# Kernel optimization log

Hardware: AMD Instinct MI355X
Metric: run time of the kernel (lower is better)

## Reference

```python
import jax, jax.numpy as jnp
import numpy as np

N_NODES = 100000
N_EDGES = 3200000
IN_DIM = 32
HID = 64


def setup_inputs() -> dict:
    key = jax.random.key(0)
    ks = jax.random.split(key, 10)
    x = jax.random.normal(ks[0], (N_NODES, IN_DIM), dtype=jnp.float32)
    edge_index = jax.random.randint(ks[1], (2, N_EDGES), 0, N_NODES, dtype=jnp.int64)
    s = 0.1
    return {
        "x": x,
        "edge_index": edge_index,
        # SAGEConv layer 1: lin_l (neighbor path, with bias), lin_r (root path, no bias)
        "w1_l": jax.random.normal(ks[2], (HID, IN_DIM), dtype=jnp.float32) * s,
        "b1_l": jnp.zeros((HID,), dtype=jnp.float32),
        "w1_r": jax.random.normal(ks[3], (HID, IN_DIM), dtype=jnp.float32) * s,
        # SAGEConv layer 2
        "w2_l": jax.random.normal(ks[4], (HID, HID), dtype=jnp.float32) * s,
        "b2_l": jnp.zeros((HID,), dtype=jnp.float32),
        "w2_r": jax.random.normal(ks[5], (HID, HID), dtype=jnp.float32) * s,
        # final classifier Linear(hidden, 1)
        "w_cls": jax.random.normal(ks[6], (1, HID), dtype=jnp.float32) * s,
        "b_cls": jnp.zeros((1,), dtype=jnp.float32),
    }


def _sage_conv(h, src, dst, n_nodes, w_l, b_l, w_r):
    # mean-aggregate neighbor features (src -> dst), then lin_l(agg) + lin_r(h)
    msg = h[src]                                   # [E, F] gather
    agg = jax.ops.segment_sum(msg, dst, num_segments=n_nodes)
    cnt = jax.ops.segment_sum(jnp.ones((src.shape[0],), h.dtype), dst,
                              num_segments=n_nodes)
    mean = agg / jnp.maximum(cnt, 1.0)[:, None]    # [N, F]
    return mean @ w_l.T + b_l + h @ w_r.T


def reference(x, edge_index, w1_l, b1_l, w1_r, w2_l, b2_l, w2_r, w_cls, b_cls):
    src, dst = edge_index[0], edge_index[1]
    n = x.shape[0]
    h = _sage_conv(x, src, dst, n, w1_l, b1_l, w1_r)
    h = jax.nn.relu(h)  # dropout is identity at inference
    h = _sage_conv(h, src, dst, n, w2_l, b2_l, w2_r)
    h = jax.nn.relu(h)
    logits = h @ w_cls.T + b_cls                   # [N, 1]
    return jnp.squeeze(logits, -1)                 # [N]
```

## Files before the change

### kernel.cpp

```cpp
#include <hip/hip_runtime.h>

#define N_NODES 100000
#define N_EDGES 3200000
#define IN_DIM 32
#define HID 64
#define BSHIFT 8
#define BNODES 256
#define NB ((N_NODES + BNODES - 1) / BNODES)
#define NWG 256
#define CHUNK (N_EDGES / NWG)
#define XBLOCKS ((N_NODES * IN_DIM + 255) / 256)

typedef unsigned short u16;
typedef unsigned char u8;
typedef _Float16 h2 __attribute__((ext_vector_type(2)));
typedef _Float16 half8 __attribute__((ext_vector_type(8)));
typedef float float4v __attribute__((ext_vector_type(4)));
typedef float f32x2 __attribute__((ext_vector_type(2)));

__device__ __forceinline__ h2 as_h2(unsigned u) {
  return __builtin_bit_cast(h2, u);
}
__device__ __forceinline__ unsigned as_u(h2 v) {
  return __builtin_bit_cast(unsigned, v);
}
__device__ __forceinline__ h2 shfl_xor_h2(h2 v, int m) {
  int i = __builtin_bit_cast(int, v);
  i = __shfl_xor(i, m, 64);
  return __builtin_bit_cast(h2, i);
}
__device__ __forceinline__ f32x2 shfl_xor_f2(f32x2 v, int m) {
  f32x2 r;
  r.x = __shfl_xor(v.x, m, 64);
  r.y = __shfl_xor(v.y, m, 64);
  return r;
}
__device__ __forceinline__ u16 f2h(float f) {
  _Float16 h = (_Float16)f;
  return __builtin_bit_cast(u16, h);
}
__device__ __forceinline__ unsigned scale_h2(unsigned u, float rinv) {
  h2 v = as_h2(u);
  h2 o;
  o.x = (_Float16)((float)v.x * rinv);
  o.y = (_Float16)((float)v.y * rinv);
  return as_u(o);
}
__device__ __forceinline__ unsigned pack2_h(float a, float b) {
  h2 o;
  o.x = (_Float16)a;
  o.y = (_Float16)b;
  return as_u(o);
}

__global__ __launch_bounds__(256) void csr_count(
    const int* __restrict__ dst, int* __restrict__ counts,
    const float* __restrict__ x, u16* __restrict__ xh, u8* __restrict__ xq,
    const float* __restrict__ w1l, const float* __restrict__ w1r,
    const float* __restrict__ w2l, const float* __restrict__ w2r,
    u16* __restrict__ w1lf, u16* __restrict__ w1rf,
    u16* __restrict__ w2lf, u16* __restrict__ w2rf) {
  int b = blockIdx.x, tid = threadIdx.x;
  if (b < NWG) {
    __shared__ int h[NB];
    for (int i = tid; i < NB; i += 256) h[i] = 0;
    __syncthreads();
    const int4* d4 = (const int4*)(dst + b * CHUNK);
    for (int i = tid; i < CHUNK / 4; i += 256) {
      int4 v = d4[i];
      atomicAdd(&h[v.x >> BSHIFT], 1);
      atomicAdd(&h[v.y >> BSHIFT], 1);
      atomicAdd(&h[v.z >> BSHIFT], 1);
      atomicAdd(&h[v.w >> BSHIFT], 1);
    }
    __syncthreads();
    for (int i = tid; i < NB; i += 256) counts[i * NWG + b] = h[i];
  } else if (b < NWG + XBLOCKS) {
    int i = (b - NWG) * 256 + tid;
    if (i < N_NODES * IN_DIM) {
      float v = x[i];
      xh[i] = f2h(v);
      int enc = __builtin_amdgcn_cvt_pk_fp8_f32(v, v, 0, false);
      xq[i] = (u8)(enc & 0xff);
    }
  } else {
    for (int i = tid; i < HID * IN_DIM; i += 256) {
      w1lf[i] = f2h(w1l[i]);
      w1rf[i] = f2h(w1r[i]);
    }
    for (int i = tid; i < HID * HID; i += 256) {
      w2lf[i] = f2h(w2l[i]);
      w2rf[i] = f2h(w2r[i]);
    }
  }
}

__global__ __launch_bounds__(256) void csr_scan_w(
    int* __restrict__ counts, int* __restrict__ btot) {
  __shared__ int s[256];
  int b = blockIdx.x, tid = threadIdx.x;
  int v = counts[b * NWG + tid];
  s[tid] = v;
  __syncthreads();
  for (int off = 1; off < 256; off <<= 1) {
    int t = (tid >= off) ? s[tid - off] : 0;
    __syncthreads();
    s[tid] += t;
    __syncthreads();
  }
  counts[b * NWG + tid] = s[tid] - v;
  if (tid == 255) btot[b] = s[255];
}

__global__ __launch_bounds__(256) void csr_scan_b(
    const int* __restrict__ btot, int* __restrict__ bbase) {
  __shared__ int s[256];
  int tid = threadIdx.x;
  int g0 = tid * 2, g1 = tid * 2 + 1;
  int v0 = (g0 < NB) ? btot[g0] : 0;
  int v1 = (g1 < NB) ? btot[g1] : 0;
  int tsum = v0 + v1;
  s[tid] = tsum;
  __syncthreads();
  for (int off = 1; off < 256; off <<= 1) {
    int t = (tid >= off) ? s[tid - off] : 0;
    __syncthreads();
    s[tid] += t;
    __syncthreads();
  }
  int run = s[tid] - tsum;
  if (g0 < NB) bbase[g0] = run;
  if (g1 < NB) bbase[g1] = run + v0;
  if (tid == 0) bbase[NB] = N_EDGES;
}

__global__ __launch_bounds__(256) void csr_place(
    const int* __restrict__ src, const int* __restrict__ dst,
    const int* __restrict__ counts, const int* __restrict__ bbase,
    unsigned* __restrict__ staged) {
  __shared__ int cur[NB];
  int w = blockIdx.x, tid = threadIdx.x;
  for (int i = tid; i < NB; i += 256) cur[i] = bbase[i] + counts[i * NWG + w];
  __syncthreads();
  const int4* d4 = (const int4*)(dst + w * CHUNK);
  const int4* s4 = (const int4*)(src + w * CHUNK);
  for (int i = tid; i < CHUNK / 4; i += 256) {
    int4 d = d4[i];
    int4 sv = s4[i];
    int p0 = atomicAdd(&cur[d.x >> BSHIFT], 1);
    staged[p0] = ((unsigned)sv.x << 8) | (unsigned)(d.x & (BNODES - 1));
    int p1 = atomicAdd(&cur[d.y >> BSHIFT], 1);
    staged[p1] = ((unsigned)sv.y << 8) | (unsigned)(d.y & (BNODES - 1));
    int p2 = atomicAdd(&cur[d.z >> BSHIFT], 1);
    staged[p2] = ((unsigned)sv.z << 8) | (unsigned)(d.z & (BNODES - 1));
    int p3 = atomicAdd(&cur[d.w >> BSHIFT], 1);
    staged[p3] = ((unsigned)sv.w << 8) | (unsigned)(d.w & (BNODES - 1));
  }
}

__global__ __launch_bounds__(256) void csr_fill(
    const unsigned* __restrict__ staged, const int* __restrict__ bbase,
    int* __restrict__ row_ptr, int* __restrict__ sorted_src) {
  __shared__ int s_cnt[BNODES];
  __shared__ int s_scan[BNODES];
  int b = blockIdx.x, tid = threadIdx.x;
  int n0 = b << BSHIFT;
  int beg = bbase[b], end = bbase[b + 1];
  s_cnt[tid] = 0;
  __syncthreads();
  for (int i = beg + tid; i < end; i += 256)
    atomicAdd(&s_cnt[staged[i] & (BNODES - 1)], 1);
  __syncthreads();
  int v = s_cnt[tid];
  s_scan[tid] = v;
  __syncthreads();
  for (int off = 1; off < BNODES; off <<= 1) {
    int t = (tid >= off) ? s_scan[tid - off] : 0;
    __syncthreads();
    s_scan[tid] += t;
    __syncthreads();
  }
  int excl = s_scan[tid] - v;
  int node = n0 + tid;
  if (node < N_NODES) row_ptr[node] = beg + excl;
  if (b == 0 && tid == 0) row_ptr[N_NODES] = N_EDGES;
  s_cnt[tid] = excl;
  __syncthreads();
  for (int i = beg + tid; i < end; i += 256) {
    unsigned p = staged[i];
    int r = atomicAdd(&s_cnt[p & (BNODES - 1)], 1);
    sorted_src[beg + r] = (int)(p >> 8);
  }
}

#define F1 72
__global__ __launch_bounds__(256) void layer1_fused(
    const u16* __restrict__ xh, const u8* __restrict__ xq,
    const int* __restrict__ row_ptr, const int* __restrict__ sorted_src,
    const u16* __restrict__ w_lf, const float* __restrict__ b_l,
    const u16* __restrict__ w_rf, u16* __restrict__ h1h,
    u8* __restrict__ h1q) {
  __shared__ __align__(16) u16 s_feat[16 * F1];

  int tid = threadIdx.x;
  int w = tid >> 6, lane = tid & 63;
  int q = lane & 3, g = lane >> 2;

  for (int m = 0; m < 4; ++m) {
    int nl = 4 * w + m;
    int node = blockIdx.x * 16 + nl;
    int rs = row_ptr[node];
    int deg = row_ptr[node + 1] - rs;
    f32x2 A0{}, A1{}, A2{}, A3{};
    f32x2 B0{}, B1{}, B2{}, B3{};
    int kk = g;
    for (; kk + 16 < deg; kk += 32) {
      int s0 = sorted_src[rs + kk];
      int s1 = sorted_src[rs + kk + 16];
      uint2 u0 = *(const uint2*)&xq[s0 * IN_DIM + 8 * q];
      uint2 u1 = *(const uint2*)&xq[s1 * IN_DIM + 8 * q];
      A0 += __builtin_amdgcn_cvt_pk_f32_fp8(u0.x, false);
      A1 += __builtin_amdgcn_cvt_pk_f32_fp8(u0.x, true);
      A2 += __builtin_amdgcn_cvt_pk_f32_fp8(u0.y, false);
      A3 += __builtin_amdgcn_cvt_pk_f32_fp8(u0.y, true);
      B0 += __builtin_amdgcn_cvt_pk_f32_fp8(u1.x, false);
      B1 += __builtin_amdgcn_cvt_pk_f32_fp8(u1.x, true);
      B2 += __builtin_amdgcn_cvt_pk_f32_fp8(u1.y, false);
      B3 += __builtin_amdgcn_cvt_pk_f32_fp8(u1.y, true);
    }
    if (kk < deg) {
      int s0 = sorted_src[rs + kk];
      uint2 u0 = *(const uint2*)&xq[s0 * IN_DIM + 8 * q];
      A0 += __builtin_amdgcn_cvt_pk_f32_fp8(u0.x, false);
      A1 += __builtin_amdgcn_cvt_pk_f32_fp8(u0.x, true);
      A2 += __builtin_amdgcn_cvt_pk_f32_fp8(u0.y, false);
      A3 += __builtin_amdgcn_cvt_pk_f32_fp8(u0.y, true);
    }
    A0 += B0; A1 += B1; A2 += B2; A3 += B3;
    h2 p0 = as_h2(pack2_h(A0.x, A0.y));
    h2 p1 = as_h2(pack2_h(A1.x, A1.y));
    h2 p2 = as_h2(pack2_h(A2.x, A2.y));
    h2 p3 = as_h2(pack2_h(A3.x, A3.y));
#pragma unroll
    for (int off = 4; off < 64; off <<= 1) {
      p0 += shfl_xor_h2(p0, off);
      p1 += shfl_xor_h2(p1, off);
      p2 += shfl_xor_h2(p2, off);
      p3 += shfl_xor_h2(p3, off);
    }
    if (g == 0) {
      float rinv = 1.0f / fmaxf((float)deg, 1.0f);
      uint4 o;
      o.x = scale_h2(as_u(p0), rinv);
      o.y = scale_h2(as_u(p1), rinv);
      o.z = scale_h2(as_u(p2), rinv);
      o.w = scale_h2(as_u(p3), rinv);
      *(uint4*)&s_feat[nl * F1 + 8 * q] = o;
    }
  }
  {
    int nm = lane >> 4, q2 = lane & 15;
    int nl = 4 * w + nm;
    int node = blockIdx.x * 16 + nl;
    unsigned ux = *(const unsigned*)&xh[node * IN_DIM + 2 * q2];
    *(unsigned*)&s_feat[nl * F1 + IN_DIM + 2 * q2] = ux;
  }
  __syncthreads();

  int q16 = lane & 15, g4 = lane >> 4;
  int j = 16 * w + q16;
  half8 b0f = *(const half8*)&w_lf[j * IN_DIM + 8 * g4];
  half8 b1f = *(const half8*)&w_rf[j * IN_DIM + 8 * g4];
  half8 a0f = *(const half8*)&s_feat[q16 * F1 + 8 * g4];
  half8 a1f = *(const half8*)&s_feat[q16 * F1 + 32 + 8 * g4];
  float4v acc = {};
  acc = __builtin_amdgcn_mfma_f32_16x16x32_f16(a0f, b0f, acc, 0, 0, 0);
  acc = __builtin_amdgcn_mfma_f32_16x16x32_f16(a1f, b1f, acc, 0, 0, 0);
  float bj = b_l[j];
#pragma unroll
  for (int reg = 0; reg < 4; ++reg) {
    int nl = 4 * g4 + reg;
    float v = fmaxf(acc[reg] + bj, 0.0f);
    int node = blockIdx.x * 16 + nl;
    h1h[node * HID + j] = f2h(v);
    int enc = __builtin_amdgcn_cvt_pk_fp8_f32(v, v, 0, false);
    h1q[node * HID + j] = (u8)(enc & 0xff);
  }
}

#define F2 136
__global__ __launch_bounds__(256) void layer2_fused(
    const u16* __restrict__ h1h, const u8* __restrict__ h1q,
    const int* __restrict__ row_ptr, const int* __restrict__ sorted_src,
    const u16* __restrict__ w_lf, const float* __restrict__ b_l,
    const u16* __restrict__ w_rf, const float* __restrict__ wc,
    const float* __restrict__ bc, float* __restrict__ out) {
  __shared__ __align__(16) u16 s_feat[16 * F2];
  __shared__ float s_out[16];

  int tid = threadIdx.x;
  if (tid < 16) s_out[tid] = bc[0];

  int w = tid >> 6, lane = tid & 63;
  int q = lane & 7, g = lane >> 3;

  for (int m = 0; m < 4; ++m) {
    int nl = 4 * w + m;
    int node = blockIdx.x * 16 + nl;
    int rs = row_ptr[node];
    int deg = row_ptr[node + 1] - rs;
    f32x2 a0{}, a1{}, a2{}, a3{};
    f32x2 b0{}, b1{}, b2{}, b3{};
    int kk = g;
    for (; kk + 8 < deg; kk += 16) {
      int s0 = sorted_src[rs + kk];
      int s1 = sorted_src[rs + kk + 8];
      uint2 u0 = *(const uint2*)&h1q[s0 * HID + 8 * q];
      uint2 u1 = *(const uint2*)&h1q[s1 * HID + 8 * q];
      a0 += __builtin_amdgcn_cvt_pk_f32_fp8(u0.x, false);
      a1 += __builtin_amdgcn_cvt_pk_f32_fp8(u0.x, true);
      a2 += __builtin_amdgcn_cvt_pk_f32_fp8(u0.y, false);
      a3 += __builtin_amdgcn_cvt_pk_f32_fp8(u0.y, true);
      b0 += __builtin_amdgcn_cvt_pk_f32_fp8(u1.x, false);
      b1 += __builtin_amdgcn_cvt_pk_f32_fp8(u1.x, true);
      b2 += __builtin_amdgcn_cvt_pk_f32_fp8(u1.y, false);
      b3 += __builtin_amdgcn_cvt_pk_f32_fp8(u1.y, true);
    }
    if (kk < deg) {
      int s0 = sorted_src[rs + kk];
      uint2 u0 = *(const uint2*)&h1q[s0 * HID + 8 * q];
      a0 += __builtin_amdgcn_cvt_pk_f32_fp8(u0.x, false);
      a1 += __builtin_amdgcn_cvt_pk_f32_fp8(u0.x, true);
      a2 += __builtin_amdgcn_cvt_pk_f32_fp8(u0.y, false);
      a3 += __builtin_amdgcn_cvt_pk_f32_fp8(u0.y, true);
    }
    a0 += b0; a1 += b1; a2 += b2; a3 += b3;
#pragma unroll
    for (int off = 8; off < 64; off <<= 1) {
      a0 += shfl_xor_f2(a0, off);
      a1 += shfl_xor_f2(a1, off);
      a2 += shfl_xor_f2(a2, off);
      a3 += shfl_xor_f2(a3, off);
    }
    if (g == 0) {
      float rinv = 1.0f / fmaxf((float)deg, 1.0f);
      uint4 o;
      o.x = pack2_h(a0.x * rinv, a0.y * rinv);
      o.y = pack2_h(a1.x * rinv, a1.y * rinv);
      o.z = pack2_h(a2.x * rinv, a2.y * rinv);
      o.w = pack2_h(a3.x * rinv, a3.y * rinv);
      *(uint4*)&s_feat[nl * F2 + 8 * q] = o;
    }
  }
  {
    int nm = lane >> 4, q2 = lane & 15;
    int nl = 4 * w + nm;
    int node = blockIdx.x * 16 + nl;
    uint2 uh = *(const uint2*)&h1h[node * HID + 4 * q2];
    *(uint2*)&s_feat[nl * F2 + HID + 4 * q2] = uh;
  }
  __syncthreads();

  int q16 = lane & 15, g4 = lane >> 4;
  int j = 16 * w + q16;
  half8 bf0 = *(const half8*)&w_lf[j * HID + 8 * g4];
  half8 bf1 = *(const half8*)&w_lf[j * HID + 32 + 8 * g4];
  half8 bf2 = *(const half8*)&w_rf[j * HID + 8 * g4];
  half8 bf3 = *(const half8*)&w_rf[j * HID + 32 + 8 * g4];
  float4v acc = {};
  acc = __builtin_amdgcn_mfma_f32_16x16x32_f16(
      *(const half8*)&s_feat[q16 * F2 + 8 * g4], bf0, acc, 0, 0, 0);
  acc = __builtin_amdgcn_mfma_f32_16x16x32_f16(
      *(const half8*)&s_feat[q16 * F2 + 32 + 8 * g4], bf1, acc, 0, 0, 0);
  acc = __builtin_amdgcn_mfma_f32_16x16x32_f16(
      *(const half8*)&s_feat[q16 * F2 + 64 + 8 * g4], bf2, acc, 0, 0, 0);
  acc = __builtin_amdgcn_mfma_f32_16x16x32_f16(
      *(const half8*)&s_feat[q16 * F2 + 96 + 8 * g4], bf3, acc, 0, 0, 0);
  float bj = b_l[j];
  float wcj = wc[j];
#pragma unroll
  for (int reg = 0; reg < 4; ++reg) {
    float v = fmaxf(acc[reg] + bj, 0.0f) * wcj;
    v += __shfl_xor(v, 1, 64);
    v += __shfl_xor(v, 2, 64);
    v += __shfl_xor(v, 4, 64);
    v += __shfl_xor(v, 8, 64);
    if (q16 == 0) atomicAdd(&s_out[4 * g4 + reg], v);
  }
  __syncthreads();
  if (tid < 16) out[blockIdx.x * 16 + tid] = s_out[tid];
}

extern "C" void kernel_launch(void* const* d_in, const int* in_sizes, int n_in,
                              void* d_out, int out_size, void* d_ws, size_t ws_size,
                              hipStream_t stream) {
  const float* x   = (const float*)d_in[0];
  const int*   ei  = (const int*)d_in[1];
  const float* w1l = (const float*)d_in[2];
  const float* b1l = (const float*)d_in[3];
  const float* w1r = (const float*)d_in[4];
  const float* w2l = (const float*)d_in[5];
  const float* b2l = (const float*)d_in[6];
  const float* w2r = (const float*)d_in[7];
  const float* wc  = (const float*)d_in[8];
  const float* bc  = (const float*)d_in[9];
  float* out = (float*)d_out;

  const int* src = ei;
  const int* dst = ei + N_EDGES;

  char* ws = (char*)d_ws;
  int*      row_ptr    = (int*)(ws + 0);
  int*      counts     = (int*)(ws + 400128);
  int*      btot       = (int*)(ws + 800768);
  int*      bbase      = (int*)(ws + 802560);
  unsigned* staged     = (unsigned*)(ws + 804352);
  int*      sorted_src = (int*)(ws + 13604352);
  u16*      xh         = (u16*)(ws + 26404352);
  u16*      h1h        = (u16*)(ws + 32804352);
  u8*       h1q        = (u8*)(ws + 45604352);
  u8*       xq         = (u8*)(ws + 52004352);
  u16*      w1lf       = (u16*)(ws + 55204352);
  u16*      w1rf       = (u16*)(ws + 55208448);
  u16*      w2lf       = (u16*)(ws + 55212544);
  u16*      w2rf       = (u16*)(ws + 55220736);

  csr_count<<<NWG + XBLOCKS + 1, 256, 0, stream>>>(
      dst, counts, x, xh, xq, w1l, w1r, w2l, w2r, w1lf, w1rf, w2lf, w2rf);
  csr_scan_w<<<NB, 256, 0, stream>>>(counts, btot);
  csr_scan_b<<<1, 256, 0, stream>>>(btot, bbase);
  csr_place<<<NWG, 256, 0, stream>>>(src, dst, counts, bbase, staged);
  csr_fill<<<NB, 256, 0, stream>>>(staged, bbase, row_ptr, sorted_src);
  layer1_fused<<<N_NODES / 16, 256, 0, stream>>>(xh, xq, row_ptr, sorted_src,
                                                 w1lf, b1l, w1rf, h1h, h1q);
  layer2_fused<<<N_NODES / 16, 256, 0, stream>>>(h1h, h1q, row_ptr, sorted_src,
                                                 w2lf, b2l, w2rf, wc, bc, out);
}
```

Measured before the change: 166.6 us.

## Split layer-1 fp8 features into two 32-column halves for cache-friendlier layer-2 gather

Layer 1 now writes its fp8 hidden features as two separate 32-byte-per-node tables, one for the low and one for the high half of the columns. Layer 2 gathers neighbours in two passes, one per half, using 4 lanes per row and 16 edges in parallel, and does the cross-lane reduction in packed fp16 instead of fp32. The aim is a smaller working set per pass (3.2 MB instead of 6.4 MB) so it fits better in cache, and cheaper shuffles. In exchange the edge index list is read twice, and summing in fp16 loses precision on high-degree nodes.

```diff
diff --git a/kernel.cpp b/kernel.cpp
--- a/kernel.cpp
+++ b/kernel.cpp
@@ -28,12 +28,6 @@
   int i = __builtin_bit_cast(int, v);
   i = __shfl_xor(i, m, 64);
   return __builtin_bit_cast(h2, i);
-}
-__device__ __forceinline__ f32x2 shfl_xor_f2(f32x2 v, int m) {
-  f32x2 r;
-  r.x = __shfl_xor(v.x, m, 64);
-  r.y = __shfl_xor(v.y, m, 64);
-  return r;
 }
 __device__ __forceinline__ u16 f2h(float f) {
   _Float16 h = (_Float16)f;
@@ -199,7 +193,7 @@
     const int* __restrict__ row_ptr, const int* __restrict__ sorted_src,
     const u16* __restrict__ w_lf, const float* __restrict__ b_l,
     const u16* __restrict__ w_rf, u16* __restrict__ h1h,
-    u8* __restrict__ h1q) {
+    u8* __restrict__ h1q_lo, u8* __restrict__ h1q_hi) {
   __shared__ __align__(16) u16 s_feat[16 * F1];
 
   int tid = threadIdx.x;
@@ -284,17 +278,22 @@
     int node = blockIdx.x * 16 + nl;
     h1h[node * HID + j] = f2h(v);
     int enc = __builtin_amdgcn_cvt_pk_fp8_f32(v, v, 0, false);
-    h1q[node * HID + j] = (u8)(enc & 0xff);
+    u8 e8 = (u8)(enc & 0xff);
+    if (j < 32)
+      h1q_lo[node * 32 + j] = e8;
+    else
+      h1q_hi[node * 32 + (j - 32)] = e8;
   }
 }
 
 #define F2 136
 __global__ __launch_bounds__(256) void layer2_fused(
-    const u16* __restrict__ h1h, const u8* __restrict__ h1q,
-    const int* __restrict__ row_ptr, const int* __restrict__ sorted_src,
-    const u16* __restrict__ w_lf, const float* __restrict__ b_l,
-    const u16* __restrict__ w_rf, const float* __restrict__ wc,
-    const float* __restrict__ bc, float* __restrict__ out) {
+    const u16* __restrict__ h1h, const u8* __restrict__ h1q_lo,
+    const u8* __restrict__ h1q_hi, const int* __restrict__ row_ptr,
+    const int* __restrict__ sorted_src, const u16* __restrict__ w_lf,
+    const float* __restrict__ b_l, const u16* __restrict__ w_rf,
+    const float* __restrict__ wc, const float* __restrict__ bc,
+    float* __restrict__ out) {
   __shared__ __align__(16) u16 s_feat[16 * F2];
   __shared__ float s_out[16];
 
@@ -302,54 +301,61 @@
   if (tid < 16) s_out[tid] = bc[0];
 
   int w = tid >> 6, lane = tid & 63;
-  int q = lane & 7, g = lane >> 3;
-
-  for (int m = 0; m < 4; ++m) {
-    int nl = 4 * w + m;
-    int node = blockIdx.x * 16 + nl;
-    int rs = row_ptr[node];
-    int deg = row_ptr[node + 1] - rs;
-    f32x2 a0{}, a1{}, a2{}, a3{};
-    f32x2 b0{}, b1{}, b2{}, b3{};
-    int kk = g;
-    for (; kk + 8 < deg; kk += 16) {
-      int s0 = sorted_src[rs + kk];
-      int s1 = sorted_src[rs + kk + 8];
-      uint2 u0 = *(const uint2*)&h1q[s0 * HID + 8 * q];
-      uint2 u1 = *(const uint2*)&h1q[s1 * HID + 8 * q];
-      a0 += __builtin_amdgcn_cvt_pk_f32_fp8(u0.x, false);
-      a1 += __builtin_amdgcn_cvt_pk_f32_fp8(u0.x, true);
-      a2 += __builtin_amdgcn_cvt_pk_f32_fp8(u0.y, false);
-      a3 += __builtin_amdgcn_cvt_pk_f32_fp8(u0.y, true);
-      b0 += __builtin_amdgcn_cvt_pk_f32_fp8(u1.x, false);
-      b1 += __builtin_amdgcn_cvt_pk_f32_fp8(u1.x, true);
-      b2 += __builtin_amdgcn_cvt_pk_f32_fp8(u1.y, false);
-      b3 += __builtin_amdgcn_cvt_pk_f32_fp8(u1.y, true);
-    }
-    if (kk < deg) {
-      int s0 = sorted_src[rs + kk];
-      uint2 u0 = *(const uint2*)&h1q[s0 * HID + 8 * q];
-      a0 += __builtin_amdgcn_cvt_pk_f32_fp8(u0.x, false);
-      a1 += __builtin_amdgcn_cvt_pk_f32_fp8(u0.x, true);
-      a2 += __builtin_amdgcn_cvt_pk_f32_fp8(u0.y, false);
-      a3 += __builtin_amdgcn_cvt_pk_f32_fp8(u0.y, true);
-    }
-    a0 += b0; a1 += b1; a2 += b2; a3 += b3;
+  int q = lane & 3, g = lane >> 2;
+
+  for (int p = 0; p < 2; ++p) {
+    const u8* tab = p ? h1q_hi : h1q_lo;
+    for (int m = 0; m < 4; ++m) {
+      int nl = 4 * w + m;
+      int node = blockIdx.x * 16 + nl;
+      int rs = row_ptr[node];
+      int deg = row_ptr[node + 1] - rs;
+      f32x2 A0{}, A1{}, A2{}, A3{};
+      f32x2 B0{}, B1{}, B2{}, B3{};
+      int kk = g;
+      for (; kk + 16 < deg; kk += 32) {
+        int s0 = sorted_src[rs + kk];
+        int s1 = sorted_src[rs + kk + 16];
+        uint2 u0 = *(const uint2*)&tab[s0 * 32 + 8 * q];
+        uint2 u1 = *(const uint2*)&tab[s1 * 32 + 8 * q];
+        A0 += __builtin_amdgcn_cvt_pk_f32_fp8(u0.x, false);
+        A1 += __builtin_amdgcn_cvt_pk_f32_fp8(u0.x, true);
+        A2 += __builtin_amdgcn_cvt_pk_f32_fp8(u0.y, false);
+        A3 += __builtin_amdgcn_cvt_pk_f32_fp8(u0.y, true);
+        B0 += __builtin_amdgcn_cvt_pk_f32_fp8(u1.x, false);
+        B1 += __builtin_amdgcn_cvt_pk_f32_fp8(u1.x, true);
+        B2 += __builtin_amdgcn_cvt_pk_f32_fp8(u1.y, false);
+        B3 += __builtin_amdgcn_cvt_pk_f32_fp8(u1.y, true);
+      }
+      if (kk < deg) {
+        int s0 = sorted_src[rs + kk];
+        uint2 u0 = *(const uint2*)&tab[s0 * 32 + 8 * q];
+        A0 += __builtin_amdgcn_cvt_pk_f32_fp8(u0.x, false);
+        A1 += __builtin_amdgcn_cvt_pk_f32_fp8(u0.x, true);
+        A2 += __builtin_amdgcn_cvt_pk_f32_fp8(u0.y, false);
+        A3 += __builtin_amdgcn_cvt_pk_f32_fp8(u0.y, true);
+      }
+      A0 += B0; A1 += B1; A2 += B2; A3 += B3;
+      h2 p0 = as_h2(pack2_h(A0.x, A0.y));
+      h2 p1 = as_h2(pack2_h(A1.x, A1.y));
+      h2 p2 = as_h2(pack2_h(A2.x, A2.y));
+      h2 p3 = as_h2(pack2_h(A3.x, A3.y));
 #pragma unroll
-    for (int off = 8; off < 64; off <<= 1) {
-      a0 += shfl_xor_f2(a0, off);
-      a1 += shfl_xor_f2(a1, off);
-      a2 += shfl_xor_f2(a2, off);
-      a3 += shfl_xor_f2(a3, off);
-    }
-    if (g == 0) {
-      float rinv = 1.0f / fmaxf((float)deg, 1.0f);
-      uint4 o;
-      o.x = pack2_h(a0.x * rinv, a0.y * rinv);
-      o.y = pack2_h(a1.x * rinv, a1.y * rinv);
-      o.z = pack2_h(a2.x * rinv, a2.y * rinv);
-      o.w = pack2_h(a3.x * rinv, a3.y * rinv);
-      *(uint4*)&s_feat[nl * F2 + 8 * q] = o;
+      for (int off = 4; off < 64; off <<= 1) {
+        p0 += shfl_xor_h2(p0, off);
+        p1 += shfl_xor_h2(p1, off);
+        p2 += shfl_xor_h2(p2, off);
+        p3 += shfl_xor_h2(p3, off);
+      }
+      if (g == 0) {
+        float rinv = 1.0f / fmaxf((float)deg, 1.0f);
+        uint4 o;
+        o.x = scale_h2(as_u(p0), rinv);
+        o.y = scale_h2(as_u(p1), rinv);
+        o.z = scale_h2(as_u(p2), rinv);
+        o.w = scale_h2(as_u(p3), rinv);
+        *(uint4*)&s_feat[nl * F2 + 32 * p + 8 * q] = o;
+      }
     }
   }
   {
@@ -418,7 +424,8 @@
   int*      sorted_src = (int*)(ws + 13604352);
   u16*      xh         = (u16*)(ws + 26404352);
   u16*      h1h        = (u16*)(ws + 32804352);
-  u8*       h1q        = (u8*)(ws + 45604352);
+  u8*       h1q_lo     = (u8*)(ws + 45604352);
+  u8*       h1q_hi     = (u8*)(ws + 48804352);
   u8*       xq         = (u8*)(ws + 52004352);
   u16*      w1lf       = (u16*)(ws + 55204352);
   u16*      w1rf       = (u16*)(ws + 55208448);
@@ -432,7 +439,9 @@
   csr_place<<<NWG, 256, 0, stream>>>(src, dst, counts, bbase, staged);
   csr_fill<<<NB, 256, 0, stream>>>(staged, bbase, row_ptr, sorted_src);
   layer1_fused<<<N_NODES / 16, 256, 0, stream>>>(xh, xq, row_ptr, sorted_src,
-                                                 w1lf, b1l, w1rf, h1h, h1q);
-  layer2_fused<<<N_NODES / 16, 256, 0, stream>>>(h1h, h1q, row_ptr, sorted_src,
+                                                 w1lf, b1l, w1rf, h1h,
+                                                 h1q_lo, h1q_hi);
+  layer2_fused<<<N_NODES / 16, 256, 0, stream>>>(h1h, h1q_lo, h1q_hi,
+                                                 row_ptr, sorted_src,
                                                  w2lf, b2l, w2rf, wc, bc, out);
 }
```

After: 186.7 us. 12.1% more time.
